# Performance work log

Hardware: AMD Instinct MI355X
Metric: run time of the kernel (lower is better)

Reference implementation:

```python
import jax, jax.numpy as jnp
import numpy as np

N_ENT, N_REL, D, H, N_MID = 4096, 200, 128, 4, 9  # 1 input layer + 9 middle layers + 1 out layer
ALPHA = 0.2
NEG = -9e15


def gat_head(x, adj_mask, W, a):
    # x: [N, Fin], W: [Fin, Fout], a: [2*Fout]
    Wh = x @ W                                   # [N, Fout]
    d = Wh.shape[-1]
    f1 = Wh @ a[:d]                              # [N]
    f2 = Wh @ a[d:]                              # [N]
    e = jax.nn.leaky_relu(f1[:, None] + f2[None, :], ALPHA)  # [N, N]
    e = jnp.where(adj_mask, e, NEG)
    attn = jax.nn.softmax(e, axis=-1)
    return attn @ Wh                             # [N, Fout]


def multihead_concat(x, adj_mask, Ws, As):
    # Ws: [H, Fin, Fout], As: [H, 2*Fout] -> elu(concat over heads) [N, H*Fout]
    heads = jax.vmap(lambda W, a: gat_head(x, adj_mask, W, a))(Ws, As)  # [H, N, Fout]
    N = x.shape[0]
    return jax.nn.elu(jnp.transpose(heads, (1, 0, 2)).reshape(N, -1))


def setup_inputs() -> dict:
    key = jax.random.key(0)
    ks = jax.random.split(key, 12)
    s = 0.1
    return {
        "head": jax.random.randint(ks[0], (4096,), 0, N_ENT),
        "relation": jax.random.randint(ks[1], (4096,), 0, N_REL),
        "adj": jax.random.normal(ks[2], (N_ENT, N_ENT), dtype=jnp.float32),
        "entity_emb": jax.random.normal(ks[3], (N_ENT, D), dtype=jnp.float32) * s,
        "relation_emb": jax.random.normal(ks[4], (N_REL, D), dtype=jnp.float32) * s,
        "W0": jax.random.normal(ks[5], (H, D, D), dtype=jnp.float32) * s,
        "a0": jax.random.normal(ks[6], (H, 2 * D), dtype=jnp.float32) * s,
        "Wm": jax.random.normal(ks[7], (N_MID, H, H * D, D), dtype=jnp.float32) * s,
        "am": jax.random.normal(ks[8], (N_MID, H, 2 * D), dtype=jnp.float32) * s,
        "Wo": jax.random.normal(ks[9], (H * D, D), dtype=jnp.float32) * s,
        "ao": jax.random.normal(ks[10], (2 * D,), dtype=jnp.float32) * s,
    }


def reference(head, relation, adj, entity_emb, relation_emb, W0, a0, Wm, am, Wo, ao):
    adj_mask = adj > 0
    # layer 0: D -> H*D
    x = multihead_concat(entity_emb, adj_mask, W0, a0)
    # 9 middle layers: H*D -> H*D (identical shapes -> scan)
    def step(x, params):
        Ws, As = params
        return multihead_concat(x, adj_mask, Ws, As), None
    x, _ = jax.lax.scan(step, x, (Wm, am))
    # output layer: single head H*D -> D, elu applied after
    x = jax.nn.elu(gat_head(x, adj_mask, Wo, ao))
    head_relation_combined = entity_emb[head] + relation_emb[relation]
    return (x, head_relation_combined)
```

## Files before the change

kernel.cpp:

```cpp
#include <hip/hip_runtime.h>

typedef unsigned short u16;
typedef short bf16x8 __attribute__((ext_vector_type(8)));
typedef float f32x4 __attribute__((ext_vector_type(4)));

__device__ __forceinline__ float bf2f(unsigned v) { return __uint_as_float(v << 16); }
__device__ __forceinline__ u16 f2bf(float f) {
    unsigned u = __float_as_uint(f);
    return (u16)((u + 0x7fffu + ((u >> 16) & 1u)) >> 16);
}

__device__ __forceinline__ void gload_lds16(const void* g, void* l) {
    __builtin_amdgcn_global_load_lds(
        (const __attribute__((address_space(1))) unsigned int*)g,
        (__attribute__((address_space(3))) unsigned int*)l, 16, 0, 0);
}


__global__ __launch_bounds__(256) void k_mask(const float* __restrict__ adj,
                                              unsigned* __restrict__ mask) {
    int w = blockIdx.x * 256 + threadIdx.x;
    const float4* q = (const float4*)(adj + (size_t)w * 32);
    unsigned bits = 0u;
#pragma unroll
    for (int i = 0; i < 8; i++) {
        float4 v = q[i];
        if (v.x > 0.f) bits |= (1u << (i * 4 + 0));
        if (v.y > 0.f) bits |= (1u << (i * 4 + 1));
        if (v.z > 0.f) bits |= (1u << (i * 4 + 2));
        if (v.w > 0.f) bits |= (1u << (i * 4 + 3));
    }
    mask[w] = bits;
}

__global__ void k_trans(const float* __restrict__ in, u16* __restrict__ out, int K) {
    __shared__ float t[32][33];
    const float* src = in + (size_t)blockIdx.z * K * 128;
    u16* dst = out + (size_t)blockIdx.z * K * 128;
    int k0 = blockIdx.x * 32, n0 = blockIdx.y * 32;
    int tx = threadIdx.x, ty = threadIdx.y;
#pragma unroll
    for (int i = 0; i < 32; i += 8) t[ty + i][tx] = src[(size_t)(k0 + ty + i) * 128 + n0 + tx];
    __syncthreads();
#pragma unroll
    for (int i = 0; i < 32; i += 8) dst[(size_t)(n0 + ty + i) * K + k0 + tx] = f2bf(t[tx][ty + i]);
}

__global__ __launch_bounds__(256) void k_cvt(const float* __restrict__ in,
                                             u16* __restrict__ out) {
    int t = blockIdx.x * 256 + threadIdx.x;
    float4 v = ((const float4*)in)[t];
    uint2 o;
    o.x = (unsigned)f2bf(v.x) | ((unsigned)f2bf(v.y) << 16);
    o.y = (unsigned)f2bf(v.z) | ((unsigned)f2bf(v.w) << 16);
    ((uint2*)out)[t] = o;
}

__global__ __launch_bounds__(1024, 4) void k_proj(const u16* __restrict__ X,
                                                  const u16* __restrict__ WT,
                                                  const float* __restrict__ avec,
                                                  u16* __restrict__ WhT,
                                                  float* __restrict__ f1,
                                                  float* __restrict__ E12g, int Fin) {
    __shared__ u16 As[2][64 * 32];
    __shared__ u16 Bs[2][128 * 32];
    __shared__ float fpart[4][64][2];
    const int tid = threadIdx.x;
    const int wv = tid >> 6, lane = tid & 63;
    const int rg = wv & 3, cg = wv >> 2;
    const int c = lane & 15, quad = lane >> 4;
    const int bofs = (quad ^ ((c >> 1) & 3)) * 8;
    const int h = blockIdx.y;
    const int j0 = blockIdx.x * 64;
    const u16* Wp = WT + (size_t)h * 128 * Fin;
    const int sgr = ((lane & 3) ^ ((lane >> 3) & 3)) * 8;

#define PROJ_STAGE(buf, kb)                                                              \
    do {                                                                                 \
        if (cg == 0)                                                                     \
            gload_lds16(X + (size_t)(j0 + rg * 16 + (lane >> 2)) * Fin + (kb) + sgr,     \
                        (void*)&As[buf][rg * 16 * 32]);                                  \
        else if (cg <= 2)                                                                \
            gload_lds16(Wp + (size_t)((cg - 1) * 64 + rg * 16 + (lane >> 2)) * Fin + (kb) + sgr, \
                        (void*)&Bs[buf][((cg - 1) * 64 + rg * 16) * 32]);                \
    } while (0)

    PROJ_STAGE(0, 0);
    __syncthreads();

    f32x4 acc[2];
    acc[0] = (f32x4){0.f, 0.f, 0.f, 0.f};
    acc[1] = (f32x4){0.f, 0.f, 0.f, 0.f};

    int it = 0;
    for (int kb = 0; kb < Fin; kb += 32, it++) {
        const int cur = it & 1;
        if (kb + 32 < Fin) PROJ_STAGE(cur ^ 1, kb + 32);
        bf16x8 av = *(const bf16x8*)&As[cur][(rg * 16 + c) * 32 + bofs];
#pragma unroll
        for (int e = 0; e < 2; e++) {
            bf16x8 bv = *(const bf16x8*)&Bs[cur][((cg * 2 + e) * 16 + c) * 32 + bofs];
            acc[e] = __builtin_amdgcn_mfma_f32_16x16x32_bf16(av, bv, acc[e], 0, 0, 0);
        }
        __syncthreads();
    }

    u16* Wo = WhT + (size_t)h * 128 * 4096;
    const float* ah = avec + h * 256;
    float p1[4] = {0, 0, 0, 0}, p2[4] = {0, 0, 0, 0};
#pragma unroll
    for (int e = 0; e < 2; e++) {
        const int n = (cg * 2 + e) * 16 + c;
        float a1 = ah[n];
        float a2 = ah[128 + n];
        u16 w4[4];
#pragma unroll
        for (int r = 0; r < 4; r++) {
            float v = acc[e][r];
            w4[r] = f2bf(v);
            p1[r] += v * a1;
            p2[r] += v * a2;
        }
        uint2 pk;
        pk.x = (unsigned)w4[0] | ((unsigned)w4[1] << 16);
        pk.y = (unsigned)w4[2] | ((unsigned)w4[3] << 16);
        *(uint2*)&Wo[(size_t)n * 4096 + j0 + rg * 16 + quad * 4] = pk;
    }
#pragma unroll
    for (int off = 1; off < 16; off <<= 1) {
#pragma unroll
        for (int r = 0; r < 4; r++) {
            p1[r] += __shfl_xor(p1[r], off);
            p2[r] += __shfl_xor(p2[r], off);
        }
    }
    if (c == 0) {
#pragma unroll
        for (int r = 0; r < 4; r++) {
            fpart[cg][rg * 16 + quad * 4 + r][0] = p1[r];
            fpart[cg][rg * 16 + quad * 4 + r][1] = p2[r];
        }
    }
    __syncthreads();
    if (tid < 64) {
        float s1 = fpart[0][tid][0] + fpart[1][tid][0] + fpart[2][tid][0] + fpart[3][tid][0];
        float s2 = fpart[0][tid][1] + fpart[1][tid][1] + fpart[2][tid][1] + fpart[3][tid][1];
        f1[h * 4096 + j0 + tid] = s1;
        const float LOG2E = 1.4426950408889634f;
        float d = s2 * LOG2E;
        float* e12 = E12g + h * 8192 + 2 * (j0 + tid);
        e12[0] = __builtin_amdgcn_exp2f(d);
        e12[1] = __builtin_amdgcn_exp2f(0.2f * d);
    }
}

template <bool F32OUT>
__global__ __launch_bounds__(1024, 4) void k_attn(const u16* __restrict__ WhT,
                                                  const float* __restrict__ f1g,
                                                  const float* __restrict__ E12g,
                                                  const unsigned char* __restrict__ maskb,
                                                  void* __restrict__ outp, int ostride) {
    __shared__ unsigned char ms[64 * 528];
    __shared__ u16 Bs[2][4][128 * 32];
    __shared__ float lpart[4][64];

    const int tid = threadIdx.x;
    const int wv = tid >> 6, lane = tid & 63;
    const int jg = wv >> 2, rg = wv & 3;
    const int c = lane & 15, quad = lane >> 4;
    const int bofs = (quad ^ ((c >> 1) & 3)) * 8;
    const int sgr = ((lane & 3) ^ ((lane >> 3) & 3)) * 8;
    const int h = blockIdx.y;
    const int i0 = blockIdx.x * 64;
    const float LOG2E = 1.4426950408889634f;
    const u16* Wp = WhT + (size_t)h * 128 * 4096;

#define ATTN_STAGE(buf, kb)                                                              \
    do {                                                                                 \
        const int jb_ = jg * 1024 + (kb) * 32;                                           \
        _Pragma("unroll")                                                                \
        for (int e_ = 0; e_ < 2; e_++)                                                   \
            gload_lds16(Wp + (size_t)(rg * 32 + e_ * 16 + (lane >> 2)) * 4096 + jb_ + sgr, \
                        (void*)&Bs[buf][jg][(rg * 32 + e_ * 16) * 32]);                  \
    } while (0)

    {
        const uint4* msrc = (const uint4*)(maskb + (size_t)i0 * 512);
#pragma unroll
        for (int e = 0; e < 2; e++) {
            int o = tid + e * 1024;
            uint4 v = msrc[o];
            int row = o >> 5, col = o & 31;
            *(uint4*)&ms[row * 528 + col * 16] = v;
        }
    }
    ATTN_STAGE(0, 0);

    const int iloc = rg * 16 + c;
    const float rf1 = f1g[h * 4096 + i0 + iloc] * LOG2E;
    const float rm = fmaxf(rf1, 0.2f * rf1);
    const float C1 = __builtin_amdgcn_exp2f(rf1 - rm);
    const float C2 = __builtin_amdgcn_exp2f(0.2f * rf1 - rm);
    const float T  = __builtin_amdgcn_exp2f(-rf1);

    const float* ep = E12g + h * 8192 + jg * 2048 + quad * 16;
    float4 eA[4], eB[4];
#pragma unroll
    for (int q = 0; q < 4; q++) eA[q] = *(const float4*)(ep + 0 * 64 + q * 4);
#pragma unroll
    for (int q = 0; q < 4; q++) eB[q] = *(const float4*)(ep + 1 * 64 + q * 4);

    bf16x8 onesv;
#pragma unroll
    for (int i = 0; i < 8; i++) onesv[i] = (short)0x3F80;

    f32x4 acc[8];
#pragma unroll
    for (int i = 0; i < 8; i++) acc[i] = (f32x4){0.f, 0.f, 0.f, 0.f};
    f32x4 acc_l = (f32x4){0.f, 0.f, 0.f, 0.f};

    union AF { bf16x8 v; unsigned u[4]; };
    AF afA, afB;

#define COMP_P(dst, mb_, E_)                                                             \
    do {                                                                                 \
        _Pragma("unroll")                                                                \
        for (int t = 0; t < 8; t += 2) {                                                 \
            float4 e_ = E_[t >> 1];                                                      \
            float p0 = ((e_.x > T) ? C1 : C2) * ((e_.x > T) ? e_.x : e_.y);              \
            float p1 = ((e_.z > T) ? C1 : C2) * ((e_.z > T) ? e_.z : e_.w);              \
            unsigned u0 = ((mb_ >> t) & 1u)       ? (__float_as_uint(p0) & 0xffff0000u) : 0u; \
            unsigned u1 = ((mb_ >> (t + 1)) & 1u) ? (__float_as_uint(p1) & 0xffff0000u) : 0u; \
            dst.u[t >> 1] = (u0 >> 16) | u1;                                             \
        }                                                                                \
    } while (0)

#define DO_MFMA(src, buf)                                                                \
    do {                                                                                 \
        _Pragma("unroll")                                                                \
        for (int nt = 0; nt < 8; nt++) {                                                 \
            bf16x8 bv_ = *(const bf16x8*)&Bs[buf][jg][(nt * 16 + c) * 32 + bofs];        \
            acc[nt] = __builtin_amdgcn_mfma_f32_16x16x32_bf16(src.v, bv_, acc[nt], 0, 0, 0); \
        }                                                                                \
        acc_l = __builtin_amdgcn_mfma_f32_16x16x32_bf16(src.v, onesv, acc_l, 0, 0, 0);   \
    } while (0)

    const unsigned char* mrow = &ms[iloc * 528 + jg * 128 + quad];
    __syncthreads();

    for (int kb = 0; kb < 32; kb += 2) {
        ATTN_STAGE(1, kb + 1);
        {
            const unsigned mbA = mrow[kb * 4];
            COMP_P(afA, mbA, eA);
        }
        if (kb + 2 < 32) {
#pragma unroll
            for (int q = 0; q < 4; q++) eA[q] = *(const float4*)(ep + (kb + 2) * 64 + q * 4);
        }
        DO_MFMA(afA, 0);
        __syncthreads();
        if (kb + 2 < 32) ATTN_STAGE(0, kb + 2);
        {
            const unsigned mbB = mrow[(kb + 1) * 4];
            COMP_P(afB, mbB, eB);
        }
        if (kb + 3 < 32) {
#pragma unroll
            for (int q = 0; q < 4; q++) eB[q] = *(const float4*)(ep + (kb + 3) * 64 + q * 4);
        }
        DO_MFMA(afB, 1);
        __syncthreads();
    }

    if (c == 0) {
#pragma unroll
        for (int r = 0; r < 4; r++)
            lpart[jg][rg * 16 + quad * 4 + r] = acc_l[r];
    }

    float* red = (float*)&Bs[0][0][0];
#pragma unroll
    for (int g = 0; g < 4; g++) {
        __syncthreads();
        if (jg == g) {
#pragma unroll
            for (int nt = 0; nt < 8; nt++) {
#pragma unroll
                for (int r = 0; r < 4; r++) {
                    int idx = (rg * 16 + quad * 4 + r) * 132 + nt * 16 + c;
                    if (g == 0) red[idx] = acc[nt][r];
                    else        red[idx] += acc[nt][r];
                }
            }
        }
    }
    __syncthreads();

    const int row = tid >> 4, cb = tid & 15;
    const float l = lpart[0][row] + lpart[1][row] + lpart[2][row] + lpart[3][row];
    const float linv = 1.0f / l;
    float vv[8];
#pragma unroll
    for (int t = 0; t < 8; t++) {
        float v = red[row * 132 + cb * 8 + t] * linv;
        vv[t] = v > 0.f ? v : __expf(v) - 1.f;
    }
    const size_t obase = (size_t)(i0 + row) * ostride + h * 128 + cb * 8;
    if (F32OUT) {
        float* op = (float*)outp + obase;
        *(float4*)op = *(float4*)&vv[0];
        *(float4*)(op + 4) = *(float4*)&vv[4];
    } else {
        uint4 o;
        o.x = (unsigned)f2bf(vv[0]) | ((unsigned)f2bf(vv[1]) << 16);
        o.y = (unsigned)f2bf(vv[2]) | ((unsigned)f2bf(vv[3]) << 16);
        o.z = (unsigned)f2bf(vv[4]) | ((unsigned)f2bf(vv[5]) << 16);
        o.w = (unsigned)f2bf(vv[6]) | ((unsigned)f2bf(vv[7]) << 16);
        *(uint4*)((u16*)outp + obase) = o;
    }
}

__global__ __launch_bounds__(256) void k_gather(const int* __restrict__ head,
                                                const int* __restrict__ rel,
                                                const float* __restrict__ ent,
                                                const float* __restrict__ rele,
                                                float* __restrict__ out) {
    int t = blockIdx.x * 256 + threadIdx.x;
    int row = t >> 5, sg = t & 31;
    int hh = head[row], rr = rel[row];
    float4 a = ((const float4*)(ent + (size_t)hh * 128))[sg];
    float4 b = ((const float4*)(rele + (size_t)rr * 128))[sg];
    float4 o;
    o.x = a.x + b.x; o.y = a.y + b.y; o.z = a.z + b.z; o.w = a.w + b.w;
    ((float4*)(out + (size_t)row * 128))[sg] = o;
}

extern "C" void kernel_launch(void* const* d_in, const int* in_sizes, int n_in,
                              void* d_out, int out_size, void* d_ws, size_t ws_size,
                              hipStream_t stream) {
    const int*   head = (const int*)d_in[0];
    const int*   rel  = (const int*)d_in[1];
    const float* adj  = (const float*)d_in[2];
    const float* ent  = (const float*)d_in[3];
    const float* rele = (const float*)d_in[4];
    const float* W0   = (const float*)d_in[5];
    const float* a0   = (const float*)d_in[6];
    const float* Wm   = (const float*)d_in[7];
    const float* am   = (const float*)d_in[8];
    const float* Wo   = (const float*)d_in[9];
    const float* ao   = (const float*)d_in[10];

    char* ws = (char*)d_ws;
    unsigned* mask = (unsigned*)(ws + 0);
    u16* WT0 = (u16*)(ws + 2097152);
    u16* WT5 = (u16*)(ws + 2228224);
    u16* WhT = (u16*)(ws + 7077888);
    float* f1 = (float*)(ws + 11272192);
    u16* xA = (u16*)(ws + 11403264);
    u16* xB = (u16*)(ws + 15597568);
    u16* x0 = (u16*)(ws + 19791872);
    float* E12 = (float*)(ws + 20840448);

    float* out_x = (float*)d_out;
    float* out_comb = out_x + (size_t)4096 * 128;

    k_mask<<<2048, 256, 0, stream>>>(adj, mask);
    k_cvt<<<512, 256, 0, stream>>>(ent, x0);
    k_trans<<<dim3(4, 4, 4), dim3(32, 8), 0, stream>>>(W0, WT0, 128);
    k_trans<<<dim3(16, 4, 36), dim3(32, 8), 0, stream>>>(Wm, WT5, 512);
    k_trans<<<dim3(16, 4, 1), dim3(32, 8), 0, stream>>>(Wo, WT5 + (size_t)36 * 512 * 128, 512);
    k_gather<<<512, 256, 0, stream>>>(head, rel, ent, rele, out_comb);

    k_proj<<<dim3(64, 4), 1024, 0, stream>>>(x0, WT0, a0, WhT, f1, E12, 128);
    k_attn<false><<<dim3(64, 4), 1024, 0, stream>>>(WhT, f1, E12, (const unsigned char*)mask, xA, 512);
    u16 *xc = xA, *xn = xB;
    for (int l = 0; l < 9; l++) {
        k_proj<<<dim3(64, 4), 1024, 0, stream>>>(xc, WT5 + (size_t)l * 4 * 512 * 128,
                                                 am + (size_t)l * 4 * 256, WhT, f1, E12, 512);
        k_attn<false><<<dim3(64, 4), 1024, 0, stream>>>(WhT, f1, E12, (const unsigned char*)mask, xn, 512);
        u16* t = xc; xc = xn; xn = t;
    }
    k_proj<<<dim3(64, 1), 1024, 0, stream>>>(xc, WT5 + (size_t)36 * 512 * 128, ao, WhT, f1, E12, 512);
    k_attn<true><<<dim3(64, 1), 1024, 0, stream>>>(WhT, f1, E12, (const unsigned char*)mask, out_x, 128);
}
```

Before: 748.4 us.

## Rewrite attention kernel with fp16 packed probabilities and global max stabilisation

Switches Wh storage and the attention MFMA from bf16 to fp16. The per-row two-branch exp selection is replaced by packed half2 multiplies and maxes. A per-head global max of f2 is computed with an atomicMax in the projection kernel so the exponentials fit fp16 range. The attention kernel is restructured to 512 threads, with each wave covering 64 rows over its own column slice, per-wave double-buffered LDS staging without block barriers, and an XCD-aware block remap. Risks include fp16 overflow or underflow in the exponentials and extra register pressure from the four accumulator sets.

```diff
diff --git a/kernel.cpp b/kernel.cpp
--- a/kernel.cpp
+++ b/kernel.cpp
@@ -1,13 +1,18 @@
 #include <hip/hip_runtime.h>
+#include <hip/hip_fp16.h>
 
 typedef unsigned short u16;
 typedef short bf16x8 __attribute__((ext_vector_type(8)));
+typedef _Float16 half8 __attribute__((ext_vector_type(8)));
 typedef float f32x4 __attribute__((ext_vector_type(4)));
 
-__device__ __forceinline__ float bf2f(unsigned v) { return __uint_as_float(v << 16); }
 __device__ __forceinline__ u16 f2bf(float f) {
     unsigned u = __float_as_uint(f);
     return (u16)((u + 0x7fffu + ((u >> 16) & 1u)) >> 16);
+}
+__device__ __forceinline__ u16 f2h(float f) {
+    __half h = __float2half_rn(f);
+    return *reinterpret_cast<u16*>(&h);
 }
 
 __device__ __forceinline__ void gload_lds16(const void* g, void* l) {
@@ -16,9 +21,9 @@
         (__attribute__((address_space(3))) unsigned int*)l, 16, 0, 0);
 }
 
-
 __global__ __launch_bounds__(256) void k_mask(const float* __restrict__ adj,
-                                              unsigned* __restrict__ mask) {
+                                              unsigned* __restrict__ mask,
+                                              int* __restrict__ slots) {
     int w = blockIdx.x * 256 + threadIdx.x;
     const float4* q = (const float4*)(adj + (size_t)w * 32);
     unsigned bits = 0u;
@@ -31,6 +36,7 @@
         if (v.w > 0.f) bits |= (1u << (i * 4 + 3));
     }
     mask[w] = bits;
+    if (blockIdx.x == 0 && threadIdx.x < 64) slots[threadIdx.x] = (int)0x80000000;
 }
 
 __global__ void k_trans(const float* __restrict__ in, u16* __restrict__ out, int K) {
@@ -61,7 +67,8 @@
                                                   const float* __restrict__ avec,
                                                   u16* __restrict__ WhT,
                                                   float* __restrict__ f1,
-                                                  float* __restrict__ E12g, int Fin) {
+                                                  float* __restrict__ E12g,
+                                                  int* __restrict__ fsl, int Fin) {
     __shared__ u16 As[2][64 * 32];
     __shared__ u16 Bs[2][128 * 32];
     __shared__ float fpart[4][64][2];
@@ -117,7 +124,7 @@
 #pragma unroll
         for (int r = 0; r < 4; r++) {
             float v = acc[e][r];
-            w4[r] = f2bf(v);
+            w4[r] = f2h(v);
             p1[r] += v * a1;
             p2[r] += v * a2;
         }
@@ -151,173 +158,245 @@
         float* e12 = E12g + h * 8192 + 2 * (j0 + tid);
         e12[0] = __builtin_amdgcn_exp2f(d);
         e12[1] = __builtin_amdgcn_exp2f(0.2f * d);
+        float dm = d;
+#pragma unroll
+        for (int off = 1; off < 64; off <<= 1) dm = fmaxf(dm, __shfl_xor(dm, off));
+        if (tid == 0) {
+            int b = __float_as_int(dm);
+            atomicMax(fsl + h, b >= 0 ? b : (b ^ 0x7fffffff));
+        }
     }
 }
 
 template <bool F32OUT>
-__global__ __launch_bounds__(1024, 4) void k_attn(const u16* __restrict__ WhT,
-                                                  const float* __restrict__ f1g,
-                                                  const float* __restrict__ E12g,
-                                                  const unsigned char* __restrict__ maskb,
-                                                  void* __restrict__ outp, int ostride) {
-    __shared__ unsigned char ms[64 * 528];
-    __shared__ u16 Bs[2][4][128 * 32];
-    __shared__ float lpart[4][64];
+__global__ __launch_bounds__(512, 2) void k_attn(const u16* __restrict__ WhT,
+                                                 const float* __restrict__ f1g,
+                                                 const float* __restrict__ E12g,
+                                                 const unsigned char* __restrict__ maskb,
+                                                 const int* __restrict__ fmx,
+                                                 void* __restrict__ outp, int ostride) {
+    __shared__ u16 Bs[8][2][128 * 32];
+    __shared__ unsigned EL[4096 + 8];
+    __shared__ float lpart[8][64];
 
     const int tid = threadIdx.x;
-    const int wv = tid >> 6, lane = tid & 63;
-    const int jg = wv >> 2, rg = wv & 3;
+    const int w = tid >> 6, lane = tid & 63;
     const int c = lane & 15, quad = lane >> 4;
     const int bofs = (quad ^ ((c >> 1) & 3)) * 8;
-    const int sgr = ((lane & 3) ^ ((lane >> 3) & 3)) * 8;
-    const int h = blockIdx.y;
-    const int i0 = blockIdx.x * 64;
+    const int g2 = (lane & 3) ^ ((lane >> 3) & 3);
+
+    int h, ib;
+    if (!F32OUT) {
+        int bid = blockIdx.x + (blockIdx.y << 6);
+        int xcd = bid & 7;
+        h = xcd >> 1;
+        ib = (bid >> 3) + ((xcd & 1) << 5);
+    } else { h = 0; ib = blockIdx.x; }
+    const int i0 = ib * 64;
     const float LOG2E = 1.4426950408889634f;
     const u16* Wp = WhT + (size_t)h * 128 * 4096;
 
-#define ATTN_STAGE(buf, kb)                                                              \
+    const u16* sbase = Wp + (size_t)(lane >> 2) * 4096 + w * 512 + g2 * 128;
+#pragma unroll
+    for (int e8 = 0; e8 < 8; e8++)
+        gload_lds16(sbase + (size_t)e8 * 16 * 4096, (void*)&Bs[w][0][e8 * 16 * 32]);
+    const u16* sp = sbase + 8;
+
+    int fk = fmx[h];
+    float F2MAX = __int_as_float(fk >= 0 ? fk : (fk ^ 0x7fffffff));
+    float t1 = __builtin_amdgcn_exp2f(-F2MAX);
+    float t2 = __builtin_amdgcn_exp2f(-0.2f * F2MAX);
+    {
+        int j = w * 512 + lane * 8;
+        const float4* eg = (const float4*)(E12g + h * 8192 + 2 * j);
+#pragma unroll
+        for (int m = 0; m < 4; m++) {
+            float4 v = eg[m];
+            __half2 p0 = __floats2half2_rn(v.x * t1, v.y * t2);
+            __half2 p1 = __floats2half2_rn(v.z * t1, v.w * t2);
+            EL[j + 2 * m] = *(const unsigned*)&p0;
+            EL[j + 2 * m + 1] = *(const unsigned*)&p1;
+        }
+    }
+
+    const unsigned char* mb0 = maskb + (size_t)(i0 + c) * 512 + w * 64 + quad * 16;
+    uint4 mqa = *(const uint4*)(mb0);
+    uint4 mqb = *(const uint4*)(mb0 + 16 * 512);
+    uint4 mqc = *(const uint4*)(mb0 + 32 * 512);
+    uint4 mqd = *(const uint4*)(mb0 + 48 * 512);
+    unsigned cur0 = mqa.x, s10 = mqa.y, s20 = mqa.z, s30 = mqa.w;
+    unsigned cur1 = mqb.x, s11 = mqb.y, s21 = mqb.z, s31 = mqb.w;
+    unsigned cur2 = mqc.x, s12 = mqc.y, s22 = mqc.z, s32 = mqc.w;
+    unsigned cur3 = mqd.x, s13 = mqd.y, s23 = mqd.z, s33 = mqd.w;
+
+    __half2 cp0, cp1, cp2, cp3;
+#define MKCP(dst, F)                                                                     \
     do {                                                                                 \
-        const int jb_ = jg * 1024 + (kb) * 32;                                           \
+        float rf1 = f1g[h * 4096 + i0 + (F) * 16 + c] * LOG2E;                           \
+        float zbv = rf1 + F2MAX;                                                         \
+        float rmv = fmaxf(zbv, 0.2f * zbv);                                              \
+        dst = __floats2half2_rn(__builtin_amdgcn_exp2f(zbv - rmv),                       \
+                                __builtin_amdgcn_exp2f(0.2f * zbv - rmv));               \
+    } while (0)
+    MKCP(cp0, 0); MKCP(cp1, 1); MKCP(cp2, 2); MKCP(cp3, 3);
+
+    half8 ones;
+#pragma unroll
+    for (int i = 0; i < 8; i++) ones[i] = (_Float16)1.0f;
+
+    f32x4 acc0[8], acc1[8], acc2[8], acc3[8];
+#pragma unroll
+    for (int i = 0; i < 8; i++) {
+        acc0[i] = (f32x4){0.f, 0.f, 0.f, 0.f};
+        acc1[i] = (f32x4){0.f, 0.f, 0.f, 0.f};
+        acc2[i] = (f32x4){0.f, 0.f, 0.f, 0.f};
+        acc3[i] = (f32x4){0.f, 0.f, 0.f, 0.f};
+    }
+    f32x4 al0 = (f32x4){0.f, 0.f, 0.f, 0.f}, al1 = al0, al2 = al0, al3 = al0;
+
+    int eoff = w * 512 + quad * 128;
+    uint4 epA0 = *(const uint4*)&EL[eoff];
+    uint4 epA1 = *(const uint4*)&EL[eoff + 4];
+    uint4 epB0, epB1;
+    eoff += 8;
+
+    asm volatile("s_waitcnt vmcnt(0)" ::: "memory");
+    __builtin_amdgcn_sched_barrier(0);
+
+#define COMPF(dst, curw, cpf, U)                                                         \
+    do {                                                                                 \
+        const unsigned mbv = ((curw) >> (8 * (U))) & 0xffu;                              \
         _Pragma("unroll")                                                                \
-        for (int e_ = 0; e_ < 2; e_++)                                                   \
-            gload_lds16(Wp + (size_t)(rg * 32 + e_ * 16 + (lane >> 2)) * 4096 + jb_ + sgr, \
-                        (void*)&Bs[buf][jg][(rg * 32 + e_ * 16) * 32]);                  \
+        for (int t = 0; t < 4; t++) {                                                    \
+            __half2 e0 = *(const __half2*)&ed[2 * t];                                    \
+            __half2 e1 = *(const __half2*)&ed[2 * t + 1];                                \
+            __half2 pr0 = __hmul2(e0, (cpf));                                            \
+            __half2 pr1 = __hmul2(e1, (cpf));                                            \
+            __half m0 = __hmax(__low2half(pr0), __high2half(pr0));                       \
+            __half m1 = __hmax(__low2half(pr1), __high2half(pr1));                       \
+            __half2 pk2 = __halves2half2(m0, m1);                                        \
+            unsigned msk = (((mbv >> (2 * t)) & 1u) ? 0xffffu : 0u) |                    \
+                           (((mbv >> (2 * t + 1)) & 1u) ? 0xffff0000u : 0u);             \
+            dst.u[t] = (*(const unsigned*)&pk2) & msk;                                   \
+        }                                                                                \
     } while (0)
 
-    {
-        const uint4* msrc = (const uint4*)(maskb + (size_t)i0 * 512);
-#pragma unroll
-        for (int e = 0; e < 2; e++) {
-            int o = tid + e * 1024;
-            uint4 v = msrc[o];
-            int row = o >> 5, col = o & 31;
-            *(uint4*)&ms[row * 528 + col * 16] = v;
-        }
-    }
-    ATTN_STAGE(0, 0);
-
-    const int iloc = rg * 16 + c;
-    const float rf1 = f1g[h * 4096 + i0 + iloc] * LOG2E;
-    const float rm = fmaxf(rf1, 0.2f * rf1);
-    const float C1 = __builtin_amdgcn_exp2f(rf1 - rm);
-    const float C2 = __builtin_amdgcn_exp2f(0.2f * rf1 - rm);
-    const float T  = __builtin_amdgcn_exp2f(-rf1);
-
-    const float* ep = E12g + h * 8192 + jg * 2048 + quad * 16;
-    float4 eA[4], eB[4];
-#pragma unroll
-    for (int q = 0; q < 4; q++) eA[q] = *(const float4*)(ep + 0 * 64 + q * 4);
-#pragma unroll
-    for (int q = 0; q < 4; q++) eB[q] = *(const float4*)(ep + 1 * 64 + q * 4);
-
-    bf16x8 onesv;
-#pragma unroll
-    for (int i = 0; i < 8; i++) onesv[i] = (short)0x3F80;
-
-    f32x4 acc[8];
-#pragma unroll
-    for (int i = 0; i < 8; i++) acc[i] = (f32x4){0.f, 0.f, 0.f, 0.f};
-    f32x4 acc_l = (f32x4){0.f, 0.f, 0.f, 0.f};
-
-    union AF { bf16x8 v; unsigned u[4]; };
-    AF afA, afB;
-
-#define COMP_P(dst, mb_, E_)                                                             \
+#define BODY(U, BUF, NBUF, EC0, EC1, EN0, EN1)                                           \
     do {                                                                                 \
         _Pragma("unroll")                                                                \
-        for (int t = 0; t < 8; t += 2) {                                                 \
-            float4 e_ = E_[t >> 1];                                                      \
-            float p0 = ((e_.x > T) ? C1 : C2) * ((e_.x > T) ? e_.x : e_.y);              \
-            float p1 = ((e_.z > T) ? C1 : C2) * ((e_.z > T) ? e_.z : e_.w);              \
-            unsigned u0 = ((mb_ >> t) & 1u)       ? (__float_as_uint(p0) & 0xffff0000u) : 0u; \
-            unsigned u1 = ((mb_ >> (t + 1)) & 1u) ? (__float_as_uint(p1) & 0xffff0000u) : 0u; \
-            dst.u[t >> 1] = (u0 >> 16) | u1;                                             \
-        }                                                                                \
-    } while (0)
-
-#define DO_MFMA(src, buf)                                                                \
-    do {                                                                                 \
+        for (int e8 = 0; e8 < 8; e8++)                                                   \
+            gload_lds16(sp + (size_t)e8 * 16 * 4096, (void*)&Bs[w][NBUF][e8 * 16 * 32]); \
+        sp += 8;                                                                         \
+        asm volatile("s_waitcnt vmcnt(8)" ::: "memory");                                 \
+        __builtin_amdgcn_sched_barrier(0);                                               \
+        EN0 = *(const uint4*)&EL[eoff];                                                  \
+        EN1 = *(const uint4*)&EL[eoff + 4];                                              \
+        eoff += 8;                                                                       \
+        const unsigned ed[8] = {EC0.x, EC0.y, EC0.z, EC0.w, EC1.x, EC1.y, EC1.z, EC1.w}; \
+        union AF { half8 v; unsigned u[4]; } af0, af1, af2, af3;                         \
+        COMPF(af0, cur0, cp0, U);                                                        \
+        COMPF(af1, cur1, cp1, U);                                                        \
+        COMPF(af2, cur2, cp2, U);                                                        \
+        COMPF(af3, cur3, cp3, U);                                                        \
         _Pragma("unroll")                                                                \
         for (int nt = 0; nt < 8; nt++) {                                                 \
-            bf16x8 bv_ = *(const bf16x8*)&Bs[buf][jg][(nt * 16 + c) * 32 + bofs];        \
-            acc[nt] = __builtin_amdgcn_mfma_f32_16x16x32_bf16(src.v, bv_, acc[nt], 0, 0, 0); \
+            half8 bv = *(const half8*)&Bs[w][BUF][(nt * 16 + c) * 32 + bofs];            \
+            acc0[nt] = __builtin_amdgcn_mfma_f32_16x16x32_f16(af0.v, bv, acc0[nt], 0, 0, 0); \
+            acc1[nt] = __builtin_amdgcn_mfma_f32_16x16x32_f16(af1.v, bv, acc1[nt], 0, 0, 0); \
+            acc2[nt] = __builtin_amdgcn_mfma_f32_16x16x32_f16(af2.v, bv, acc2[nt], 0, 0, 0); \
+            acc3[nt] = __builtin_amdgcn_mfma_f32_16x16x32_f16(af3.v, bv, acc3[nt], 0, 0, 0); \
         }                                                                                \
-        acc_l = __builtin_amdgcn_mfma_f32_16x16x32_bf16(src.v, onesv, acc_l, 0, 0, 0);   \
+        al0 = __builtin_amdgcn_mfma_f32_16x16x32_f16(af0.v, ones, al0, 0, 0, 0);         \
+        al1 = __builtin_amdgcn_mfma_f32_16x16x32_f16(af1.v, ones, al1, 0, 0, 0);         \
+        al2 = __builtin_amdgcn_mfma_f32_16x16x32_f16(af2.v, ones, al2, 0, 0, 0);         \
+        al3 = __builtin_amdgcn_mfma_f32_16x16x32_f16(af3.v, ones, al3, 0, 0, 0);         \
     } while (0)
 
-    const unsigned char* mrow = &ms[iloc * 528 + jg * 128 + quad];
-    __syncthreads();
-
-    for (int kb = 0; kb < 32; kb += 2) {
-        ATTN_STAGE(1, kb + 1);
-        {
-            const unsigned mbA = mrow[kb * 4];
-            COMP_P(afA, mbA, eA);
-        }
-        if (kb + 2 < 32) {
-#pragma unroll
-            for (int q = 0; q < 4; q++) eA[q] = *(const float4*)(ep + (kb + 2) * 64 + q * 4);
-        }
-        DO_MFMA(afA, 0);
-        __syncthreads();
-        if (kb + 2 < 32) ATTN_STAGE(0, kb + 2);
-        {
-            const unsigned mbB = mrow[(kb + 1) * 4];
-            COMP_P(afB, mbB, eB);
-        }
-        if (kb + 3 < 32) {
-#pragma unroll
-            for (int q = 0; q < 4; q++) eB[q] = *(const float4*)(ep + (kb + 3) * 64 + q * 4);
-        }
-        DO_MFMA(afB, 1);
-        __syncthreads();
+    for (int s = 0; s < 4; s++) {
+        BODY(0, 0, 1, epA0, epA1, epB0, epB1);
+        BODY(1, 1, 0, epB0, epB1, epA0, epA1);
+        BODY(2, 0, 1, epA0, epA1, epB0, epB1);
+        BODY(3, 1, 0, epB0, epB1, epA0, epA1);
+        cur0 = s10; s10 = s20; s20 = s30;
+        cur1 = s11; s11 = s21; s21 = s31;
+        cur2 = s12; s12 = s22; s22 = s32;
+        cur3 = s13; s13 = s23; s23 = s33;
     }
 
     if (c == 0) {
 #pragma unroll
-        for (int r = 0; r < 4; r++)
-            lpart[jg][rg * 16 + quad * 4 + r] = acc_l[r];
-    }
-
-    float* red = (float*)&Bs[0][0][0];
-#pragma unroll
-    for (int g = 0; g < 4; g++) {
-        __syncthreads();
-        if (jg == g) {
-#pragma unroll
-            for (int nt = 0; nt < 8; nt++) {
-#pragma unroll
-                for (int r = 0; r < 4; r++) {
-                    int idx = (rg * 16 + quad * 4 + r) * 132 + nt * 16 + c;
-                    if (g == 0) red[idx] = acc[nt][r];
-                    else        red[idx] += acc[nt][r];
-                }
-            }
-        }
-    }
-    __syncthreads();
-
-    const int row = tid >> 4, cb = tid & 15;
-    const float l = lpart[0][row] + lpart[1][row] + lpart[2][row] + lpart[3][row];
+        for (int r = 0; r < 4; r++) {
+            lpart[w][0 * 16 + quad * 4 + r] = al0[r];
+            lpart[w][1 * 16 + quad * 4 + r] = al1[r];
+            lpart[w][2 * 16 + quad * 4 + r] = al2[r];
+            lpart[w][3 * 16 + quad * 4 + r] = al3[r];
+        }
+    }
+    __syncthreads();
+
+    float* redb = (float*)&Bs[0][0][0];
+#define DUMPQ(A, F)                                                                      \
+    _Pragma("unroll") for (int nt = 0; nt < 8; nt++)                                     \
+    _Pragma("unroll") for (int r = 0; r < 4; r++)                                        \
+        rq[((F) * 16 + quad * 4 + r) * 128 + nt * 16 + c] = A[nt][r];
+#define ADDQ(A, F)                                                                       \
+    _Pragma("unroll") for (int nt = 0; nt < 8; nt++)                                     \
+    _Pragma("unroll") for (int r = 0; r < 4; r++)                                        \
+        rq[((F) * 16 + quad * 4 + r) * 128 + nt * 16 + c] += A[nt][r];
+    if (w >= 4) {
+        float* rq = redb + (w - 4) * 8192;
+        DUMPQ(acc0, 0) DUMPQ(acc1, 1) DUMPQ(acc2, 2) DUMPQ(acc3, 3)
+    }
+    __syncthreads();
+    if (w < 4) {
+        float* rq = redb + w * 8192;
+        ADDQ(acc0, 0) ADDQ(acc1, 1) ADDQ(acc2, 2) ADDQ(acc3, 3)
+    }
+    __syncthreads();
+    {
+        f32x4* r0 = (f32x4*)redb;
+        f32x4* r1 = (f32x4*)(redb + 8192);
+        f32x4* r2 = (f32x4*)(redb + 16384);
+        f32x4* r3 = (f32x4*)(redb + 24576);
+        for (int t = tid; t < 2048; t += 512) { r0[t] += r2[t]; r1[t] += r3[t]; }
+    }
+    __syncthreads();
+
+    const int row = tid >> 3, ob = tid & 7;
+    float l = 0.f;
+#pragma unroll
+    for (int g = 0; g < 8; g++) l += lpart[g][row];
     const float linv = 1.0f / l;
-    float vv[8];
-#pragma unroll
-    for (int t = 0; t < 8; t++) {
-        float v = red[row * 132 + cb * 8 + t] * linv;
-        vv[t] = v > 0.f ? v : __expf(v) - 1.f;
-    }
-    const size_t obase = (size_t)(i0 + row) * ostride + h * 128 + cb * 8;
+    float vv[16];
+#pragma unroll
+    for (int half = 0; half < 2; half++) {
+#pragma unroll
+        for (int t = 0; t < 8; t++) {
+            int idx = row * 128 + (ob + half * 8) * 8 + t;
+            float v = (redb[idx] + redb[8192 + idx]) * linv;
+            vv[half * 8 + t] = v > 0.f ? v : __expf(v) - 1.f;
+        }
+    }
+    const size_t obase = (size_t)(i0 + row) * ostride + h * 128 + ob * 8;
     if (F32OUT) {
         float* op = (float*)outp + obase;
         *(float4*)op = *(float4*)&vv[0];
         *(float4*)(op + 4) = *(float4*)&vv[4];
+        *(float4*)(op + 64) = *(float4*)&vv[8];
+        *(float4*)(op + 68) = *(float4*)&vv[12];
     } else {
+        u16* op = (u16*)outp + obase;
         uint4 o;
         o.x = (unsigned)f2bf(vv[0]) | ((unsigned)f2bf(vv[1]) << 16);
         o.y = (unsigned)f2bf(vv[2]) | ((unsigned)f2bf(vv[3]) << 16);
         o.z = (unsigned)f2bf(vv[4]) | ((unsigned)f2bf(vv[5]) << 16);
         o.w = (unsigned)f2bf(vv[6]) | ((unsigned)f2bf(vv[7]) << 16);
-        *(uint4*)((u16*)outp + obase) = o;
+        *(uint4*)op = o;
+        o.x = (unsigned)f2bf(vv[8])  | ((unsigned)f2bf(vv[9]) << 16);
+        o.y = (unsigned)f2bf(vv[10]) | ((unsigned)f2bf(vv[11]) << 16);
+        o.z = (unsigned)f2bf(vv[12]) | ((unsigned)f2bf(vv[13]) << 16);
+        o.w = (unsigned)f2bf(vv[14]) | ((unsigned)f2bf(vv[15]) << 16);
+        *(uint4*)(op + 64) = o;
     }
 }
 
@@ -361,26 +440,32 @@
     u16* xB = (u16*)(ws + 15597568);
     u16* x0 = (u16*)(ws + 19791872);
     float* E12 = (float*)(ws + 20840448);
+    int* slots = (int*)(ws + 20971520);
 
     float* out_x = (float*)d_out;
     float* out_comb = out_x + (size_t)4096 * 128;
 
-    k_mask<<<2048, 256, 0, stream>>>(adj, mask);
+    k_mask<<<2048, 256, 0, stream>>>(adj, mask, slots);
     k_cvt<<<512, 256, 0, stream>>>(ent, x0);
     k_trans<<<dim3(4, 4, 4), dim3(32, 8), 0, stream>>>(W0, WT0, 128);
     k_trans<<<dim3(16, 4, 36), dim3(32, 8), 0, stream>>>(Wm, WT5, 512);
     k_trans<<<dim3(16, 4, 1), dim3(32, 8), 0, stream>>>(Wo, WT5 + (size_t)36 * 512 * 128, 512);
     k_gather<<<512, 256, 0, stream>>>(head, rel, ent, rele, out_comb);
 
-    k_proj<<<dim3(64, 4), 1024, 0, stream>>>(x0, WT0, a0, WhT, f1, E12, 128);
-    k_attn<false><<<dim3(64, 4), 1024, 0, stream>>>(WhT, f1, E12, (const unsigned char*)mask, xA, 512);
+    k_proj<<<dim3(64, 4), 1024, 0, stream>>>(x0, WT0, a0, WhT, f1, E12, slots, 128);
+    k_attn<false><<<dim3(64, 4), 512, 0, stream>>>(WhT, f1, E12, (const unsigned char*)mask,
+                                                   slots, xA, 512);
     u16 *xc = xA, *xn = xB;
     for (int l = 0; l < 9; l++) {
         k_proj<<<dim3(64, 4), 1024, 0, stream>>>(xc, WT5 + (size_t)l * 4 * 512 * 128,
-                                                 am + (size_t)l * 4 * 256, WhT, f1, E12, 512);
-        k_attn<false><<<dim3(64, 4), 1024, 0, stream>>>(WhT, f1, E12, (const unsigned char*)mask, xn, 512);
+                                                 am + (size_t)l * 4 * 256, WhT, f1, E12,
+                                                 slots + (l + 1) * 4, 512);
+        k_attn<false><<<dim3(64, 4), 512, 0, stream>>>(WhT, f1, E12, (const unsigned char*)mask,
+                                                       slots + (l + 1) * 4, xn, 512);
         u16* t = xc; xc = xn; xn = t;
     }
-    k_proj<<<dim3(64, 1), 1024, 0, stream>>>(xc, WT5 + (size_t)36 * 512 * 128, ao, WhT, f1, E12, 512);
-    k_attn<true><<<dim3(64, 1), 1024, 0, stream>>>(WhT, f1, E12, (const unsigned char*)mask, out_x, 128);
-}
+    k_proj<<<dim3(64, 1), 1024, 0, stream>>>(xc, WT5 + (size_t)36 * 512 * 128, ao, WhT, f1, E12,
+                                             slots + 40, 512);
+    k_attn<true><<<dim3(64, 1), 512, 0, stream>>>(WhT, f1, E12, (const unsigned char*)mask,
+                                                  slots + 40, out_x, 128);
+}
```

New measurement: 1.298 ms. +73.4%, slower.

## Switch attention to fp16 MFMA with global-max softmax shift and 2-row-block waves

Applied to the files above, without the earlier changes.

Wh is now stored as fp16 instead of bf16, and the attention kernel uses f16 MFMA. Probabilities are computed in half2 arithmetic using a per-head global max of f2, which the projection kernel gathers through atomicMax into workspace slots. The attention kernel is restructured so each wave handles two 16-row fragments (32 rows) over a 512-column slice. It reads mask words straight from global memory instead of staging them in LDS, and precomputes scaled exp factors in LDS. This cuts per-element float exp/select work and reuses each B fragment across two MFMAs. The costs are more LDS, a wider cross-wave reduction, and fp16 overflow/underflow risk in the probabilities.

```diff
diff --git a/kernel.cpp b/kernel.cpp
--- a/kernel.cpp
+++ b/kernel.cpp
@@ -1,13 +1,18 @@
 #include <hip/hip_runtime.h>
+#include <hip/hip_fp16.h>
 
 typedef unsigned short u16;
 typedef short bf16x8 __attribute__((ext_vector_type(8)));
+typedef _Float16 half8 __attribute__((ext_vector_type(8)));
 typedef float f32x4 __attribute__((ext_vector_type(4)));
 
-__device__ __forceinline__ float bf2f(unsigned v) { return __uint_as_float(v << 16); }
 __device__ __forceinline__ u16 f2bf(float f) {
     unsigned u = __float_as_uint(f);
     return (u16)((u + 0x7fffu + ((u >> 16) & 1u)) >> 16);
+}
+__device__ __forceinline__ u16 f2h(float f) {
+    __half h = __float2half_rn(f);
+    return *reinterpret_cast<u16*>(&h);
 }
 
 __device__ __forceinline__ void gload_lds16(const void* g, void* l) {
@@ -16,9 +21,9 @@
         (__attribute__((address_space(3))) unsigned int*)l, 16, 0, 0);
 }
 
-
 __global__ __launch_bounds__(256) void k_mask(const float* __restrict__ adj,
-                                              unsigned* __restrict__ mask) {
+                                              unsigned* __restrict__ mask,
+                                              int* __restrict__ slots) {
     int w = blockIdx.x * 256 + threadIdx.x;
     const float4* q = (const float4*)(adj + (size_t)w * 32);
     unsigned bits = 0u;
@@ -31,6 +36,7 @@
         if (v.w > 0.f) bits |= (1u << (i * 4 + 3));
     }
     mask[w] = bits;
+    if (blockIdx.x == 0 && threadIdx.x < 64) slots[threadIdx.x] = (int)0x80000000;
 }
 
 __global__ void k_trans(const float* __restrict__ in, u16* __restrict__ out, int K) {
@@ -61,7 +67,8 @@
                                                   const float* __restrict__ avec,
                                                   u16* __restrict__ WhT,
                                                   float* __restrict__ f1,
-                                                  float* __restrict__ E12g, int Fin) {
+                                                  float* __restrict__ E12g,
+                                                  int* __restrict__ fsl, int Fin) {
     __shared__ u16 As[2][64 * 32];
     __shared__ u16 Bs[2][128 * 32];
     __shared__ float fpart[4][64][2];
@@ -117,7 +124,7 @@
 #pragma unroll
         for (int r = 0; r < 4; r++) {
             float v = acc[e][r];
-            w4[r] = f2bf(v);
+            w4[r] = f2h(v);
             p1[r] += v * a1;
             p2[r] += v * a2;
         }
@@ -151,6 +158,13 @@
         float* e12 = E12g + h * 8192 + 2 * (j0 + tid);
         e12[0] = __builtin_amdgcn_exp2f(d);
         e12[1] = __builtin_amdgcn_exp2f(0.2f * d);
+        float dm = d;
+#pragma unroll
+        for (int off = 1; off < 64; off <<= 1) dm = fmaxf(dm, __shfl_xor(dm, off));
+        if (tid == 0) {
+            int b = __float_as_int(dm);
+            atomicMax(fsl + h, b >= 0 ? b : (b ^ 0x7fffffff));
+        }
     }
 }
 
@@ -159,14 +173,17 @@
                                                   const float* __restrict__ f1g,
                                                   const float* __restrict__ E12g,
                                                   const unsigned char* __restrict__ maskb,
+                                                  const int* __restrict__ fmx,
                                                   void* __restrict__ outp, int ostride) {
-    __shared__ unsigned char ms[64 * 528];
-    __shared__ u16 Bs[2][4][128 * 32];
-    __shared__ float lpart[4][64];
+    __shared__ uint4 SMv[9344];
+    char* SM = (char*)SMv;
+    u16* Bsb = (u16*)SM;
+    unsigned* EL = (unsigned*)(SM + 131072);
+    float* lpart = (float*)(SM + 147456);
 
     const int tid = threadIdx.x;
     const int wv = tid >> 6, lane = tid & 63;
-    const int jg = wv >> 2, rg = wv & 3;
+    const int jg = wv >> 1, rg = wv & 1;
     const int c = lane & 15, quad = lane >> 4;
     const int bofs = (quad ^ ((c >> 1) & 3)) * 8;
     const int sgr = ((lane & 3) ^ ((lane >> 3) & 3)) * 8;
@@ -175,135 +192,173 @@
     const float LOG2E = 1.4426950408889634f;
     const u16* Wp = WhT + (size_t)h * 128 * 4096;
 
-#define ATTN_STAGE(buf, kb)                                                              \
+    u16* tile0 = Bsb + (jg * 2 + 0) * 4096;
+    u16* tile1 = Bsb + (jg * 2 + 1) * 4096;
+
+#define ATTN_STAGE(tbuf, kb)                                                             \
     do {                                                                                 \
-        const int jb_ = jg * 1024 + (kb) * 32;                                           \
+        const int jb_ = jg * 512 + (kb) * 32;                                            \
         _Pragma("unroll")                                                                \
-        for (int e_ = 0; e_ < 2; e_++)                                                   \
-            gload_lds16(Wp + (size_t)(rg * 32 + e_ * 16 + (lane >> 2)) * 4096 + jb_ + sgr, \
-                        (void*)&Bs[buf][jg][(rg * 32 + e_ * 16) * 32]);                  \
+        for (int e_ = 0; e_ < 4; e_++)                                                   \
+            gload_lds16(Wp + (size_t)(rg * 64 + e_ * 16 + (lane >> 2)) * 4096 + jb_ + sgr, \
+                        (void*)((tbuf) + (rg * 64 + e_ * 16) * 32));                     \
     } while (0)
 
+    ATTN_STAGE(tile0, 0);
+
+    int fk = fmx[h];
+    float F2MAX = __int_as_float(fk >= 0 ? fk : (fk ^ 0x7fffffff));
+    float t1 = __builtin_amdgcn_exp2f(-F2MAX);
+    float t2 = __builtin_amdgcn_exp2f(-0.2f * F2MAX);
     {
-        const uint4* msrc = (const uint4*)(maskb + (size_t)i0 * 512);
-#pragma unroll
-        for (int e = 0; e < 2; e++) {
-            int o = tid + e * 1024;
-            uint4 v = msrc[o];
-            int row = o >> 5, col = o & 31;
-            *(uint4*)&ms[row * 528 + col * 16] = v;
-        }
-    }
-    ATTN_STAGE(0, 0);
-
-    const int iloc = rg * 16 + c;
-    const float rf1 = f1g[h * 4096 + i0 + iloc] * LOG2E;
-    const float rm = fmaxf(rf1, 0.2f * rf1);
-    const float C1 = __builtin_amdgcn_exp2f(rf1 - rm);
-    const float C2 = __builtin_amdgcn_exp2f(0.2f * rf1 - rm);
-    const float T  = __builtin_amdgcn_exp2f(-rf1);
-
-    const float* ep = E12g + h * 8192 + jg * 2048 + quad * 16;
-    float4 eA[4], eB[4];
-#pragma unroll
-    for (int q = 0; q < 4; q++) eA[q] = *(const float4*)(ep + 0 * 64 + q * 4);
-#pragma unroll
-    for (int q = 0; q < 4; q++) eB[q] = *(const float4*)(ep + 1 * 64 + q * 4);
-
-    bf16x8 onesv;
-#pragma unroll
-    for (int i = 0; i < 8; i++) onesv[i] = (short)0x3F80;
-
-    f32x4 acc[8];
-#pragma unroll
-    for (int i = 0; i < 8; i++) acc[i] = (f32x4){0.f, 0.f, 0.f, 0.f};
-    f32x4 acc_l = (f32x4){0.f, 0.f, 0.f, 0.f};
-
-    union AF { bf16x8 v; unsigned u[4]; };
-    AF afA, afB;
-
-#define COMP_P(dst, mb_, E_)                                                             \
+        int j = tid * 4;
+        const float4* eg = (const float4*)(E12g + h * 8192 + 2 * j);
+        float4 v0 = eg[0], v1 = eg[1];
+        __half2 a0 = __floats2half2_rn(v0.x * t1, v0.y * t2);
+        __half2 a1 = __floats2half2_rn(v0.z * t1, v0.w * t2);
+        __half2 a2 = __floats2half2_rn(v1.x * t1, v1.y * t2);
+        __half2 a3 = __floats2half2_rn(v1.z * t1, v1.w * t2);
+        uint4 pk;
+        pk.x = *(unsigned*)&a0; pk.y = *(unsigned*)&a1;
+        pk.z = *(unsigned*)&a2; pk.w = *(unsigned*)&a3;
+        *(uint4*)&EL[j] = pk;
+    }
+
+    __half2 cpa, cpb;
+    {
+        float rf1 = f1g[h * 4096 + i0 + rg * 32 + c] * LOG2E;
+        float zb = rf1 + F2MAX, rm = fmaxf(zb, 0.2f * zb);
+        cpa = __floats2half2_rn(__builtin_amdgcn_exp2f(zb - rm),
+                                __builtin_amdgcn_exp2f(0.2f * zb - rm));
+    }
+    {
+        float rf1 = f1g[h * 4096 + i0 + rg * 32 + 16 + c] * LOG2E;
+        float zb = rf1 + F2MAX, rm = fmaxf(zb, 0.2f * zb);
+        cpb = __floats2half2_rn(__builtin_amdgcn_exp2f(zb - rm),
+                                __builtin_amdgcn_exp2f(0.2f * zb - rm));
+    }
+
+    const unsigned char* mpa = maskb + (size_t)(i0 + rg * 32 + c) * 512 + jg * 64;
+    const unsigned char* mpb = mpa + 16 * 512;
+
+    half8 ones;
+#pragma unroll
+    for (int i = 0; i < 8; i++) ones[i] = (_Float16)1.0f;
+
+    f32x4 accA[8], accB[8];
+#pragma unroll
+    for (int i = 0; i < 8; i++) {
+        accA[i] = (f32x4){0.f, 0.f, 0.f, 0.f};
+        accB[i] = (f32x4){0.f, 0.f, 0.f, 0.f};
+    }
+    f32x4 alA = (f32x4){0.f, 0.f, 0.f, 0.f};
+    f32x4 alB = (f32x4){0.f, 0.f, 0.f, 0.f};
+
+    union AF { half8 v; unsigned u[4]; };
+
+#define COMPF(dst, mbv, cpf)                                                             \
     do {                                                                                 \
         _Pragma("unroll")                                                                \
-        for (int t = 0; t < 8; t += 2) {                                                 \
-            float4 e_ = E_[t >> 1];                                                      \
-            float p0 = ((e_.x > T) ? C1 : C2) * ((e_.x > T) ? e_.x : e_.y);              \
-            float p1 = ((e_.z > T) ? C1 : C2) * ((e_.z > T) ? e_.z : e_.w);              \
-            unsigned u0 = ((mb_ >> t) & 1u)       ? (__float_as_uint(p0) & 0xffff0000u) : 0u; \
-            unsigned u1 = ((mb_ >> (t + 1)) & 1u) ? (__float_as_uint(p1) & 0xffff0000u) : 0u; \
-            dst.u[t >> 1] = (u0 >> 16) | u1;                                             \
+        for (int t = 0; t < 4; t++) {                                                    \
+            __half2 e0 = *(const __half2*)&ed[2 * t];                                    \
+            __half2 e1 = *(const __half2*)&ed[2 * t + 1];                                \
+            __half2 pr0 = __hmul2(e0, (cpf));                                            \
+            __half2 pr1 = __hmul2(e1, (cpf));                                            \
+            __half m0 = __hmax(__low2half(pr0), __high2half(pr0));                       \
+            __half m1 = __hmax(__low2half(pr1), __high2half(pr1));                       \
+            __half2 pk2 = __halves2half2(m0, m1);                                        \
+            unsigned msk = ((((mbv) >> (2 * t)) & 1u) ? 0xffffu : 0u) |                  \
+                           ((((mbv) >> (2 * t + 1)) & 1u) ? 0xffff0000u : 0u);           \
+            dst.u[t] = (*(const unsigned*)&pk2) & msk;                                   \
         }                                                                                \
     } while (0)
 
-#define DO_MFMA(src, buf)                                                                \
+#define STEP(kb, PAR, mwa, mwb)                                                          \
     do {                                                                                 \
+        u16* curb = (PAR) ? tile1 : tile0;                                               \
+        if ((kb) < 15) ATTN_STAGE((PAR) ? tile0 : tile1, (kb) + 1);                      \
+        uint4 ew0 = *(const uint4*)&EL[jg * 512 + (kb) * 32 + quad * 8];                 \
+        uint4 ew1 = *(const uint4*)&EL[jg * 512 + (kb) * 32 + quad * 8 + 4];             \
+        const unsigned ed[8] = {ew0.x, ew0.y, ew0.z, ew0.w, ew1.x, ew1.y, ew1.z, ew1.w}; \
+        const unsigned mbva = ((mwa) >> (8 * quad)) & 0xffu;                             \
+        const unsigned mbvb = ((mwb) >> (8 * quad)) & 0xffu;                             \
+        AF afa, afb;                                                                     \
+        COMPF(afa, mbva, cpa);                                                           \
+        COMPF(afb, mbvb, cpb);                                                           \
         _Pragma("unroll")                                                                \
         for (int nt = 0; nt < 8; nt++) {                                                 \
-            bf16x8 bv_ = *(const bf16x8*)&Bs[buf][jg][(nt * 16 + c) * 32 + bofs];        \
-            acc[nt] = __builtin_amdgcn_mfma_f32_16x16x32_bf16(src.v, bv_, acc[nt], 0, 0, 0); \
+            half8 bv = *(const half8*)&curb[(nt * 16 + c) * 32 + bofs];                  \
+            accA[nt] = __builtin_amdgcn_mfma_f32_16x16x32_f16(afa.v, bv, accA[nt], 0, 0, 0); \
+            accB[nt] = __builtin_amdgcn_mfma_f32_16x16x32_f16(afb.v, bv, accB[nt], 0, 0, 0); \
         }                                                                                \
-        acc_l = __builtin_amdgcn_mfma_f32_16x16x32_bf16(src.v, onesv, acc_l, 0, 0, 0);   \
+        alA = __builtin_amdgcn_mfma_f32_16x16x32_f16(afa.v, ones, alA, 0, 0, 0);         \
+        alB = __builtin_amdgcn_mfma_f32_16x16x32_f16(afb.v, ones, alB, 0, 0, 0);         \
+        __syncthreads();                                                                 \
     } while (0)
 
-    const unsigned char* mrow = &ms[iloc * 528 + jg * 128 + quad];
-    __syncthreads();
-
-    for (int kb = 0; kb < 32; kb += 2) {
-        ATTN_STAGE(1, kb + 1);
-        {
-            const unsigned mbA = mrow[kb * 4];
-            COMP_P(afA, mbA, eA);
-        }
-        if (kb + 2 < 32) {
-#pragma unroll
-            for (int q = 0; q < 4; q++) eA[q] = *(const float4*)(ep + (kb + 2) * 64 + q * 4);
-        }
-        DO_MFMA(afA, 0);
-        __syncthreads();
-        if (kb + 2 < 32) ATTN_STAGE(0, kb + 2);
-        {
-            const unsigned mbB = mrow[(kb + 1) * 4];
-            COMP_P(afB, mbB, eB);
-        }
-        if (kb + 3 < 32) {
-#pragma unroll
-            for (int q = 0; q < 4; q++) eB[q] = *(const float4*)(ep + (kb + 3) * 64 + q * 4);
-        }
-        DO_MFMA(afB, 1);
-        __syncthreads();
+    __syncthreads();
+
+    for (int s = 0; s < 4; s++) {
+        uint4 mca = *(const uint4*)(mpa + 16 * s);
+        uint4 mcb = *(const uint4*)(mpb + 16 * s);
+        STEP(s * 4 + 0, 0, mca.x, mcb.x);
+        STEP(s * 4 + 1, 1, mca.y, mcb.y);
+        STEP(s * 4 + 2, 0, mca.z, mcb.z);
+        STEP(s * 4 + 3, 1, mca.w, mcb.w);
     }
 
     if (c == 0) {
 #pragma unroll
-        for (int r = 0; r < 4; r++)
-            lpart[jg][rg * 16 + quad * 4 + r] = acc_l[r];
-    }
-
-    float* red = (float*)&Bs[0][0][0];
-#pragma unroll
-    for (int g = 0; g < 4; g++) {
-        __syncthreads();
-        if (jg == g) {
-#pragma unroll
-            for (int nt = 0; nt < 8; nt++) {
-#pragma unroll
-                for (int r = 0; r < 4; r++) {
-                    int idx = (rg * 16 + quad * 4 + r) * 132 + nt * 16 + c;
-                    if (g == 0) red[idx] = acc[nt][r];
-                    else        red[idx] += acc[nt][r];
-                }
+        for (int r = 0; r < 4; r++) {
+            lpart[jg * 64 + rg * 32 + quad * 4 + r] = alA[r];
+            lpart[jg * 64 + rg * 32 + 16 + quad * 4 + r] = alB[r];
+        }
+    }
+    __syncthreads();
+
+    float* Q = (float*)SM;
+#define QIDX(f, ntv, rv) ((rg * 32 + (f) * 16 + quad * 4 + (rv)) * 132 + (ntv) * 16 + c)
+    if (jg >= 4) {
+        float* rq = Q + (jg - 4) * 8448;
+#pragma unroll
+        for (int nt = 0; nt < 8; nt++)
+#pragma unroll
+            for (int r = 0; r < 4; r++) {
+                rq[QIDX(0, nt, r)] = accA[nt][r];
+                rq[QIDX(1, nt, r)] = accB[nt][r];
             }
-        }
+    }
+    __syncthreads();
+    if (jg < 4) {
+        float* rq = Q + jg * 8448;
+#pragma unroll
+        for (int nt = 0; nt < 8; nt++)
+#pragma unroll
+            for (int r = 0; r < 4; r++) {
+                rq[QIDX(0, nt, r)] += accA[nt][r];
+                rq[QIDX(1, nt, r)] += accB[nt][r];
+            }
+    }
+    __syncthreads();
+    {
+        f32x4* q0 = (f32x4*)Q;
+        f32x4* q1 = (f32x4*)(Q + 8448);
+        f32x4* q2 = (f32x4*)(Q + 16896);
+        f32x4* q3 = (f32x4*)(Q + 25344);
+        for (int t = tid; t < 2112; t += 1024) { q0[t] += q2[t]; q1[t] += q3[t]; }
     }
     __syncthreads();
 
     const int row = tid >> 4, cb = tid & 15;
-    const float l = lpart[0][row] + lpart[1][row] + lpart[2][row] + lpart[3][row];
+    float l = 0.f;
+#pragma unroll
+    for (int g = 0; g < 8; g++) l += lpart[g * 64 + row];
     const float linv = 1.0f / l;
     float vv[8];
 #pragma unroll
     for (int t = 0; t < 8; t++) {
-        float v = red[row * 132 + cb * 8 + t] * linv;
+        int idx = row * 132 + cb * 8 + t;
+        float v = (Q[idx] + Q[8448 + idx]) * linv;
         vv[t] = v > 0.f ? v : __expf(v) - 1.f;
     }
     const size_t obase = (size_t)(i0 + row) * ostride + h * 128 + cb * 8;
@@ -361,26 +416,32 @@
     u16* xB = (u16*)(ws + 15597568);
     u16* x0 = (u16*)(ws + 19791872);
     float* E12 = (float*)(ws + 20840448);
+    int* slots = (int*)(ws + 20971520);
 
     float* out_x = (float*)d_out;
     float* out_comb = out_x + (size_t)4096 * 128;
 
-    k_mask<<<2048, 256, 0, stream>>>(adj, mask);
+    k_mask<<<2048, 256, 0, stream>>>(adj, mask, slots);
     k_cvt<<<512, 256, 0, stream>>>(ent, x0);
     k_trans<<<dim3(4, 4, 4), dim3(32, 8), 0, stream>>>(W0, WT0, 128);
     k_trans<<<dim3(16, 4, 36), dim3(32, 8), 0, stream>>>(Wm, WT5, 512);
     k_trans<<<dim3(16, 4, 1), dim3(32, 8), 0, stream>>>(Wo, WT5 + (size_t)36 * 512 * 128, 512);
     k_gather<<<512, 256, 0, stream>>>(head, rel, ent, rele, out_comb);
 
-    k_proj<<<dim3(64, 4), 1024, 0, stream>>>(x0, WT0, a0, WhT, f1, E12, 128);
-    k_attn<false><<<dim3(64, 4), 1024, 0, stream>>>(WhT, f1, E12, (const unsigned char*)mask, xA, 512);
+    k_proj<<<dim3(64, 4), 1024, 0, stream>>>(x0, WT0, a0, WhT, f1, E12, slots, 128);
+    k_attn<false><<<dim3(64, 4), 1024, 0, stream>>>(WhT, f1, E12, (const unsigned char*)mask,
+                                                    slots, xA, 512);
     u16 *xc = xA, *xn = xB;
     for (int l = 0; l < 9; l++) {
         k_proj<<<dim3(64, 4), 1024, 0, stream>>>(xc, WT5 + (size_t)l * 4 * 512 * 128,
-                                                 am + (size_t)l * 4 * 256, WhT, f1, E12, 512);
-        k_attn<false><<<dim3(64, 4), 1024, 0, stream>>>(WhT, f1, E12, (const unsigned char*)mask, xn, 512);
+                                                 am + (size_t)l * 4 * 256, WhT, f1, E12,
+                                                 slots + (l + 1) * 4, 512);
+        k_attn<false><<<dim3(64, 4), 1024, 0, stream>>>(WhT, f1, E12, (const unsigned char*)mask,
+                                                        slots + (l + 1) * 4, xn, 512);
         u16* t = xc; xc = xn; xn = t;
     }
-    k_proj<<<dim3(64, 1), 1024, 0, stream>>>(xc, WT5 + (size_t)36 * 512 * 128, ao, WhT, f1, E12, 512);
-    k_attn<true><<<dim3(64, 1), 1024, 0, stream>>>(WhT, f1, E12, (const unsigned char*)mask, out_x, 128);
-}
+    k_proj<<<dim3(64, 1), 1024, 0, stream>>>(xc, WT5 + (size_t)36 * 512 * 128, ao, WhT, f1, E12,
+                                             slots + 40, 512);
+    k_attn<true><<<dim3(64, 1), 1024, 0, stream>>>(WhT, f1, E12, (const unsigned char*)mask,
+                                                   slots + 40, out_x, 128);
+}
```

Result: slower. 1.189 ms (+58.8%).
